# Optimization experiments

Measured on AMD Instinct MI355X. Metric: run time of the kernel, lower is better.

## Reference

```python
import jax, jax.numpy as jnp
import numpy as np

HIDDEN = 2048
N_HEADS = 16
HEAD_DIM = HIDDEN // N_HEADS
ROPE_THETA = 10000.0
BSZ, SEQ = 2, 2048
NEG_INF = -1e9


def setup_inputs() -> dict:
    key = jax.random.key(0)
    ks = jax.random.split(key, 5)
    scale = 1.0 / np.sqrt(HIDDEN)
    hidden_states = jax.random.normal(ks[0], (BSZ, SEQ, HIDDEN), dtype=jnp.float32)
    Wq = jax.random.normal(ks[1], (HIDDEN, HIDDEN), dtype=jnp.float32) * scale
    Wk = jax.random.normal(ks[2], (HIDDEN, HIDDEN), dtype=jnp.float32) * scale
    Wv = jax.random.normal(ks[3], (HIDDEN, HIDDEN), dtype=jnp.float32) * scale
    Wo = jax.random.normal(ks[4], (HIDDEN, HIDDEN), dtype=jnp.float32) * scale
    # additive causal mask, [1, 1, S, S]
    causal = jnp.triu(jnp.full((SEQ, SEQ), NEG_INF, dtype=jnp.float32), k=1)
    attention_mask = causal[None, None, :, :]
    position_ids = jnp.arange(SEQ, dtype=jnp.int32)
    return {
        "hidden_states": hidden_states,
        "Wq": Wq, "Wk": Wk, "Wv": Wv, "Wo": Wo,
        "attention_mask": attention_mask,
        "position_ids": position_ids,
    }


def _rotate_half(x):
    half = x.shape[-1] // 2
    return jnp.concatenate((-x[..., half:], x[..., :half]), axis=-1)


def _rope_tables(seq_len, position_ids):
    # inv_freq: [head_dim/2]
    inv_freq = 1.0 / (ROPE_THETA ** (jnp.arange(0, HEAD_DIM, 2, dtype=jnp.float32) / HEAD_DIM))
    t = jnp.arange(seq_len, dtype=jnp.float32)
    freqs = t[:, None] * inv_freq[None, :]              # [S, D/2]
    emb = jnp.concatenate((freqs, freqs), axis=-1)      # [S, D]
    cos = jnp.cos(emb)[position_ids]                    # [S, D]
    sin = jnp.sin(emb)[position_ids]
    return cos, sin


def reference(hidden_states, Wq, Wk, Wv, Wo, attention_mask, position_ids):
    b, s, h = hidden_states.shape
    def proj(W):
        return (hidden_states @ W.T).reshape(b, s, N_HEADS, HEAD_DIM).transpose(0, 2, 1, 3)
    q = proj(Wq)  # [B, H, S, D]
    k = proj(Wk)
    v = proj(Wv)
    cos, sin = _rope_tables(s, position_ids)            # [S, D], broadcasts over B,H
    q = q * cos + _rotate_half(q) * sin
    k = k * cos + _rotate_half(k) * sin
    scores = jnp.einsum('bhqd,bhkd->bhqk', q, k) / np.sqrt(HEAD_DIM)
    scores = scores + attention_mask
    w = jax.nn.softmax(scores, axis=-1)
    out = jnp.einsum('bhqk,bhkd->bhqd', w, v)           # [B, H, S, D]
    out = out.transpose(0, 2, 1, 3).reshape(b, s, h)
    return out @ Wo.T
```

## Files before the change

kernel.cpp:

```cpp
#include <hip/hip_runtime.h>
#include <cstdint>
#include <cstddef>

typedef __bf16 bf16;
typedef __bf16 bf16x4 __attribute__((ext_vector_type(4)));
typedef __bf16 bf16x8 __attribute__((ext_vector_type(8)));
typedef float  f32x4  __attribute__((ext_vector_type(4)));
typedef short  s16x4  __attribute__((ext_vector_type(4)));

#define HIDDEN 2048
#define NHEADS 16
#define HDIM   128
#define BSZ    2
#define SEQ    2048
#define BS     (BSZ*SEQ)
#define QKW    (2*HIDDEN)

union b4u { bf16x4 h; s16x4 s; };

__device__ __forceinline__ void async16(const bf16* g, bf16* l) {
    __builtin_amdgcn_global_load_lds(
        (const __attribute__((address_space(1))) unsigned int*)g,
        (__attribute__((address_space(3))) unsigned int*)l, 16, 0, 0);
}

__global__ __launch_bounds__(256) void cast_all(const float* __restrict__ hs,
                                                const float* __restrict__ Wq,
                                                const float* __restrict__ Wk,
                                                const float* __restrict__ Wv,
                                                const float* __restrict__ Wo,
                                                const int* __restrict__ pos,
                                                bf16* __restrict__ hs_b,
                                                bf16* __restrict__ wqkv,
                                                bf16* __restrict__ wo_b,
                                                float2* __restrict__ tab) {
    int i = blockIdx.x * 256 + threadIdx.x;
    if (i >= 6291456) {
        int j = i - 6291456;
        int s = j >> 6, p = j & 63;
        float t = (float)pos[s];
        float inv = expf(-(float)(2 * p) * (9.2103403719761836f / 128.0f));
        float sn, cs;
        sincosf(t * inv, &sn, &cs);
        tab[j] = make_float2(cs, sn);
        return;
    }
    const float* src; bf16* dst; int off;
    if (i < 2097152) { src = hs; dst = hs_b; off = i; }
    else {
        int j = i - 2097152;
        int r = j >> 20;
        off = j & 1048575;
        if      (r == 0) { src = Wq; dst = wqkv; }
        else if (r == 1) { src = Wk; dst = wqkv + (size_t)4194304; }
        else if (r == 2) { src = Wv; dst = wqkv + (size_t)8388608; }
        else             { src = Wo; dst = wo_b; }
    }
    const float4 v = ((const float4*)src)[off];
    bf16x4 o;
    o.x = (bf16)v.x; o.y = (bf16)v.y; o.z = (bf16)v.z; o.w = (bf16)v.w;
    ((bf16x4*)dst)[off] = o;
}

__global__ __launch_bounds__(256) void gemm_qkv(const bf16* __restrict__ A,
                                                const bf16* __restrict__ Bt,
                                                const float2* __restrict__ tab,
                                                bf16* __restrict__ qk,
                                                bf16* __restrict__ vtb) {
    __shared__ bf16 Als[128 * 32];
    __shared__ bf16 Bls[128 * 32];
    const int K    = HIDDEN;
    const int tid  = threadIdx.x;
    const int lane = tid & 63;
    const int w    = tid >> 6;
    const int l15  = lane & 15;
    const int quad = lane >> 4;
    const int mTile = blockIdx.y * 128;
    const int nTile = blockIdx.x * 128;
    const int wm = (w >> 1) * 64;
    const int wv = w & 1;

    f32x4 acc[4][4];
#pragma unroll
    for (int i = 0; i < 4; ++i)
#pragma unroll
        for (int j = 0; j < 4; ++j) acc[i][j] = (f32x4){0.f, 0.f, 0.f, 0.f};

    const bf16* gA = A + (size_t)(mTile + w * 32 + (lane >> 2)) * K + (lane & 3) * 8;
    const bf16* gB = Bt + (size_t)(nTile + w * 32 + (lane >> 2)) * K + (lane & 3) * 8;
    bf16* lA = Als + w * 1024;
    bf16* lB = Bls + w * 1024;

    for (int k0 = 0; k0 < K; k0 += 32) {
        async16(gA + k0,          lA);
        async16(gA + 16 * K + k0, lA + 512);
        async16(gB + k0,          lB);
        async16(gB + 16 * K + k0, lB + 512);
        __syncthreads();

        bf16x8 af[4], bfr[4];
#pragma unroll
        for (int mi = 0; mi < 4; ++mi)
            af[mi] = *(const bf16x8*)(Als + (wm + mi * 16 + l15) * 32 + quad * 8);
#pragma unroll
        for (int ni = 0; ni < 4; ++ni) {
            int co = wv * 32 + (ni & 1) * 16 + (ni >> 1) * 64;
            bfr[ni] = *(const bf16x8*)(Bls + (co + l15) * 32 + quad * 8);
        }
#pragma unroll
        for (int mi = 0; mi < 4; ++mi)
#pragma unroll
            for (int ni = 0; ni < 4; ++ni)
                acc[mi][ni] = __builtin_amdgcn_mfma_f32_16x16x32_bf16(
                    af[mi], bfr[ni], acc[mi][ni], 0, 0, 0);
        __syncthreads();
    }

    if (nTile < QKW) {
#pragma unroll
        for (int mi = 0; mi < 4; ++mi)
#pragma unroll
            for (int r = 0; r < 4; ++r) {
                int row = mTile + wm + mi * 16 + quad * 4 + r;
                int s   = row & (SEQ - 1);
                float2 t0 = tab[s * 64 + wv * 32 + l15];
                float2 t1 = tab[s * 64 + wv * 32 + 16 + l15];
                size_t rb = (size_t)row * QKW + nTile + wv * 32 + l15;
                float lo0 = acc[mi][0][r], hi0 = acc[mi][2][r];
                float lo1 = acc[mi][1][r], hi1 = acc[mi][3][r];
                qk[rb]      = (bf16)(lo0 * t0.x - hi0 * t0.y);
                qk[rb + 64] = (bf16)(hi0 * t0.x + lo0 * t0.y);
                qk[rb + 16] = (bf16)(lo1 * t1.x - hi1 * t1.y);
                qk[rb + 80] = (bf16)(hi1 * t1.x + lo1 * t1.y);
            }
    } else {
#pragma unroll
        for (int mi = 0; mi < 4; ++mi)
#pragma unroll
            for (int ni = 0; ni < 4; ++ni) {
                int col_v = (nTile - QKW) + wv * 32 + (ni & 1) * 16 + (ni >> 1) * 64 + l15;
                int row0  = mTile + wm + mi * 16 + quad * 4;
                bf16x4 pk;
#pragma unroll
                for (int r = 0; r < 4; ++r) pk[r] = (bf16)acc[mi][ni][r];
                *(bf16x4*)(vtb + (size_t)col_v * BS + row0) = pk;
            }
    }
}

template <typename OutT>
__global__ __launch_bounds__(256) void gemm_bt(const bf16* __restrict__ A,
                                               const bf16* __restrict__ Bt,
                                               OutT* __restrict__ C,
                                               int M, int N, int K) {
    __shared__ bf16 Als[128 * 32];
    __shared__ bf16 Bls[128 * 32];
    const int tid  = threadIdx.x;
    const int lane = tid & 63;
    const int w    = tid >> 6;
    const int l15  = lane & 15;
    const int quad = lane >> 4;
    const int mTile = blockIdx.y * 128;
    const int nTile = blockIdx.x * 128;
    const int wm = (w >> 1) * 64;
    const int wn = (w & 1) * 64;

    f32x4 acc[4][4];
#pragma unroll
    for (int i = 0; i < 4; ++i)
#pragma unroll
        for (int j = 0; j < 4; ++j) acc[i][j] = (f32x4){0.f, 0.f, 0.f, 0.f};

    const bf16* gA = A + (size_t)(mTile + w * 32 + (lane >> 2)) * K + (lane & 3) * 8;
    const bf16* gB = Bt + (size_t)(nTile + w * 32 + (lane >> 2)) * K + (lane & 3) * 8;
    bf16* lA = Als + w * 1024;
    bf16* lB = Bls + w * 1024;

    for (int k0 = 0; k0 < K; k0 += 32) {
        async16(gA + k0,          lA);
        async16(gA + 16 * K + k0, lA + 512);
        async16(gB + k0,          lB);
        async16(gB + 16 * K + k0, lB + 512);
        __syncthreads();

        bf16x8 af[4], bfr[4];
#pragma unroll
        for (int mi = 0; mi < 4; ++mi)
            af[mi] = *(const bf16x8*)(Als + (wm + mi * 16 + l15) * 32 + quad * 8);
#pragma unroll
        for (int ni = 0; ni < 4; ++ni)
            bfr[ni] = *(const bf16x8*)(Bls + (wn + ni * 16 + l15) * 32 + quad * 8);
#pragma unroll
        for (int mi = 0; mi < 4; ++mi)
#pragma unroll
            for (int ni = 0; ni < 4; ++ni)
                acc[mi][ni] = __builtin_amdgcn_mfma_f32_16x16x32_bf16(
                    af[mi], bfr[ni], acc[mi][ni], 0, 0, 0);
        __syncthreads();
    }

#pragma unroll
    for (int mi = 0; mi < 4; ++mi)
#pragma unroll
        for (int ni = 0; ni < 4; ++ni)
#pragma unroll
            for (int r = 0; r < 4; ++r) {
                int row = mTile + wm + mi * 16 + quad * 4 + r;
                int col = nTile + wn + ni * 16 + l15;
                C[(size_t)row * N + col] = (OutT)acc[mi][ni][r];
            }
}

__global__ __launch_bounds__(256) void attn_kernel(const bf16* __restrict__ qk,
                                                   const bf16* __restrict__ vt,
                                                   bf16* __restrict__ ao) {
    __shared__ bf16 Kls[64 * 128];
    __shared__ bf16 Vls[128 * 64];

    const int tid  = threadIdx.x;
    const int lane = tid & 63;
    const int w    = tid >> 6;
    const int l15  = lane & 15;
    const int quad = lane >> 4;
    const int bid  = blockIdx.x;
    const int qt   = 31 - (bid >> 5);
    const int bh   = bid & 31;
    const int b    = bh >> 4;
    const int h    = bh & 15;
    const int qbase = qt * 64;
    const size_t seq0 = (size_t)b * SEQ;

    bf16x8 qf[4];
    {
        const bf16* qp = qk + (seq0 + qbase + w * 16 + l15) * QKW + h * HDIM + quad * 8;
#pragma unroll
        for (int ks = 0; ks < 4; ++ks) qf[ks] = *(const bf16x8*)(qp + ks * 32);
    }

    f32x4 o[8];
#pragma unroll
    for (int i = 0; i < 8; ++i) o[i] = (f32x4){0.f, 0.f, 0.f, 0.f};
    float m_s = -3e38f, l_s = 0.f;
    const int qg = qbase + w * 16 + l15;

    const int krow = lane >> 4;
    const int kp   = lane & 15;
    const int vrow = lane >> 3;
    const int vp   = lane & 7;
    const int sw   = l15 & 7;

    for (int t = 0; t <= qt; ++t) {
        const int kb = t * 64;
#pragma unroll
        for (int i = 0; i < 4; ++i) {
            int j = w * 16 + i * 4 + krow;
            int c = (kp & 8) | ((kp & 7) ^ (j & 7));
            async16(qk + (seq0 + kb + j) * QKW + HIDDEN + h * HDIM + c * 8,
                    Kls + (w * 4 + i) * 512);
        }
#pragma unroll
        for (int i = 0; i < 4; ++i) {
            int d = w * 32 + i * 8 + vrow;
            int c = vp ^ (d & 7);
            async16(vt + (size_t)(h * HDIM + d) * (size_t)BS + seq0 + kb + c * 8,
                    Vls + (w * 4 + i) * 512);
        }
        __syncthreads();

        f32x4 sa[4];
#pragma unroll
        for (int ni = 0; ni < 4; ++ni) sa[ni] = (f32x4){0.f, 0.f, 0.f, 0.f};
#pragma unroll
        for (int ni = 0; ni < 4; ++ni)
#pragma unroll
            for (int ks = 0; ks < 4; ++ks) {
                bf16x8 kf = *(const bf16x8*)(Kls + (ni * 16 + l15) * 128 +
                                             (((ks * 4 + quad) ^ sw) << 3));
                sa[ni] = __builtin_amdgcn_mfma_f32_16x16x32_bf16(kf, qf[ks], sa[ni], 0, 0, 0);
            }

        const float scale = 0.08838834764831845f * 1.4426950408889634f;
        float rmax = -3e38f;
        const bool diag = (t == qt);
#pragma unroll
        for (int ni = 0; ni < 4; ++ni)
#pragma unroll
            for (int r = 0; r < 4; ++r) {
                float sv = sa[ni][r] * scale;
                if (diag) {
                    int jg = kb + ni * 16 + quad * 4 + r;
                    if (jg > qg) sv = -1e30f;
                }
                sa[ni][r] = sv;
                rmax = fmaxf(rmax, sv);
            }
        rmax = fmaxf(rmax, __shfl_xor(rmax, 16));
        rmax = fmaxf(rmax, __shfl_xor(rmax, 32));

        float mn = fmaxf(m_s, rmax);
        float alpha = exp2f(m_s - mn);
        m_s = mn;
        float rsum = 0.f;
        b4u pb[4];
#pragma unroll
        for (int ni = 0; ni < 4; ++ni)
#pragma unroll
            for (int r = 0; r < 4; ++r) {
                float e = exp2f(sa[ni][r] - mn);
                rsum += e;
                pb[ni].h[r] = (bf16)e;
            }
        rsum += __shfl_xor(rsum, 16);
        rsum += __shfl_xor(rsum, 32);
        l_s = l_s * alpha + rsum;

        if (__ballot(alpha != 1.f) != 0ull) {
#pragma unroll
            for (int n2 = 0; n2 < 8; ++n2)
#pragma unroll
                for (int r = 0; r < 4; ++r) o[n2][r] *= alpha;
        }

#pragma unroll
        for (int n2 = 0; n2 < 8; ++n2)
#pragma unroll
            for (int ni = 0; ni < 4; ++ni) {
                b4u vf;
                vf.h = *(const bf16x4*)(Vls + (n2 * 16 + l15) * 64 +
                                        ((((ni * 2 + (quad >> 1)) ^ sw) << 3) + (quad & 1) * 4));
                o[n2] = __builtin_amdgcn_mfma_f32_16x16x16bf16_1k(vf.s, pb[ni].s, o[n2], 0, 0, 0);
            }
        __syncthreads();
    }

    const float inv = 1.0f / l_s;
    bf16* op = ao + (seq0 + qg) * HIDDEN + h * HDIM + quad * 4;
#pragma unroll
    for (int n2 = 0; n2 < 8; ++n2) {
        bf16x4 pk;
#pragma unroll
        for (int r = 0; r < 4; ++r) pk[r] = (bf16)(o[n2][r] * inv);
        *(bf16x4*)(op + n2 * 16) = pk;
    }
}

extern "C" void kernel_launch(void* const* d_in, const int* in_sizes, int n_in,
                              void* d_out, int out_size, void* d_ws, size_t ws_size,
                              hipStream_t stream) {
    const float* hs = (const float*)d_in[0];
    const float* Wq = (const float*)d_in[1];
    const float* Wk = (const float*)d_in[2];
    const float* Wv = (const float*)d_in[3];
    const float* Wo = (const float*)d_in[4];
    const int* pos  = (const int*)d_in[6];
    float* out = (float*)d_out;

    bf16* hs_b = (bf16*)d_ws;
    bf16* wqkv = hs_b + (size_t)8388608;
    bf16* wo_b = wqkv + (size_t)12582912;
    bf16* qkb  = wo_b + (size_t)4194304;
    bf16* vtb  = qkb + (size_t)16777216;
    bf16* ao   = vtb + (size_t)8388608;
    float2* tab = (float2*)ao;

    cast_all<<<25088, 256, 0, stream>>>(hs, Wq, Wk, Wv, Wo, pos, hs_b, wqkv, wo_b, tab);
    gemm_qkv<<<dim3(48, 32), 256, 0, stream>>>(hs_b, wqkv, tab, qkb, vtb);
    attn_kernel<<<1024, 256, 0, stream>>>(qkb, vtb, ao);
    gemm_bt<float><<<dim3(HIDDEN / 128, BS / 128), 256, 0, stream>>>(ao, wo_b, out, BS, HIDDEN, HIDDEN);
}
```

Before: 398.8 us.

## Double GEMM K-tile with XOR-swizzled LDS; use 128-query attention blocks with 8 waves

Both GEMM kernels now stage 64-wide K slices instead of 32. The LDS layout is XOR-swizzled to avoid bank conflicts, which halves the number of barrier round-trips per output tile. The attention kernel moves from 64 to 128 query rows per block with 512 threads, so each K/V tile loaded into LDS is shared by twice as many queries. Waves whose rows lie fully above a key tile skip its compute but still take part in loads and barriers. The trade-off is more LDS per GEMM block and more idle waves on diagonal tiles in attention, which may reduce occupancy.

New measurement: 403.9 us. About the same (+1.3%).

```diff
diff --git a/kernel.cpp b/kernel.cpp
--- a/kernel.cpp
+++ b/kernel.cpp
@@ -62,19 +62,21 @@
     ((bf16x4*)dst)[off] = o;
 }
 
+
 __global__ __launch_bounds__(256) void gemm_qkv(const bf16* __restrict__ A,
                                                 const bf16* __restrict__ Bt,
                                                 const float2* __restrict__ tab,
                                                 bf16* __restrict__ qk,
                                                 bf16* __restrict__ vtb) {
-    __shared__ bf16 Als[128 * 32];
-    __shared__ bf16 Bls[128 * 32];
+    __shared__ bf16 Als[128 * 64];
+    __shared__ bf16 Bls[128 * 64];
     const int K    = HIDDEN;
     const int tid  = threadIdx.x;
     const int lane = tid & 63;
     const int w    = tid >> 6;
     const int l15  = lane & 15;
     const int quad = lane >> 4;
+    const int sw   = l15 & 7;
     const int mTile = blockIdx.y * 128;
     const int nTile = blockIdx.x * 128;
     const int wm = (w >> 1) * 64;
@@ -86,33 +88,40 @@
 #pragma unroll
         for (int j = 0; j < 4; ++j) acc[i][j] = (f32x4){0.f, 0.f, 0.f, 0.f};
 
-    const bf16* gA = A + (size_t)(mTile + w * 32 + (lane >> 2)) * K + (lane & 3) * 8;
-    const bf16* gB = Bt + (size_t)(nTile + w * 32 + (lane >> 2)) * K + (lane & 3) * 8;
-    bf16* lA = Als + w * 1024;
-    bf16* lB = Bls + w * 1024;
-
-    for (int k0 = 0; k0 < K; k0 += 32) {
-        async16(gA + k0,          lA);
-        async16(gA + 16 * K + k0, lA + 512);
-        async16(gB + k0,          lB);
-        async16(gB + 16 * K + k0, lB + 512);
-        __syncthreads();
-
-        bf16x8 af[4], bfr[4];
-#pragma unroll
-        for (int mi = 0; mi < 4; ++mi)
-            af[mi] = *(const bf16x8*)(Als + (wm + mi * 16 + l15) * 32 + quad * 8);
-#pragma unroll
-        for (int ni = 0; ni < 4; ++ni) {
-            int co = wv * 32 + (ni & 1) * 16 + (ni >> 1) * 64;
-            bfr[ni] = *(const bf16x8*)(Bls + (co + l15) * 32 + quad * 8);
-        }
-#pragma unroll
-        for (int mi = 0; mi < 4; ++mi)
-#pragma unroll
-            for (int ni = 0; ni < 4; ++ni)
-                acc[mi][ni] = __builtin_amdgcn_mfma_f32_16x16x32_bf16(
-                    af[mi], bfr[ni], acc[mi][ni], 0, 0, 0);
+    const int cOff = (((lane & 7) ^ (lane >> 3)) & 7) * 8;
+    const bf16* gA = A + (size_t)(mTile + w * 32 + (lane >> 3)) * K + cOff;
+    const bf16* gB = Bt + (size_t)(nTile + w * 32 + (lane >> 3)) * K + cOff;
+    bf16* lA = Als + w * 2048;
+    bf16* lB = Bls + w * 2048;
+    const int rstep = 8 * K;
+
+    for (int k0 = 0; k0 < K; k0 += 64) {
+#pragma unroll
+        for (int i = 0; i < 4; ++i) async16(gA + k0 + i * rstep, lA + i * 512);
+#pragma unroll
+        for (int i = 0; i < 4; ++i) async16(gB + k0 + i * rstep, lB + i * 512);
+        __syncthreads();
+
+#pragma unroll
+        for (int s = 0; s < 2; ++s) {
+            bf16x8 af[4], bfr[4];
+#pragma unroll
+            for (int mi = 0; mi < 4; ++mi)
+                af[mi] = *(const bf16x8*)(Als + (wm + mi * 16 + l15) * 64 +
+                                          (((s * 4 + quad) ^ sw) << 3));
+#pragma unroll
+            for (int ni = 0; ni < 4; ++ni) {
+                int co = wv * 32 + (ni & 1) * 16 + (ni >> 1) * 64;
+                bfr[ni] = *(const bf16x8*)(Bls + (co + l15) * 64 +
+                                           (((s * 4 + quad) ^ sw) << 3));
+            }
+#pragma unroll
+            for (int mi = 0; mi < 4; ++mi)
+#pragma unroll
+                for (int ni = 0; ni < 4; ++ni)
+                    acc[mi][ni] = __builtin_amdgcn_mfma_f32_16x16x32_bf16(
+                        af[mi], bfr[ni], acc[mi][ni], 0, 0, 0);
+        }
         __syncthreads();
     }
 
@@ -153,13 +162,14 @@
                                                const bf16* __restrict__ Bt,
                                                OutT* __restrict__ C,
                                                int M, int N, int K) {
-    __shared__ bf16 Als[128 * 32];
-    __shared__ bf16 Bls[128 * 32];
+    __shared__ bf16 Als[128 * 64];
+    __shared__ bf16 Bls[128 * 64];
     const int tid  = threadIdx.x;
     const int lane = tid & 63;
     const int w    = tid >> 6;
     const int l15  = lane & 15;
     const int quad = lane >> 4;
+    const int sw   = l15 & 7;
     const int mTile = blockIdx.y * 128;
     const int nTile = blockIdx.x * 128;
     const int wm = (w >> 1) * 64;
@@ -171,31 +181,38 @@
 #pragma unroll
         for (int j = 0; j < 4; ++j) acc[i][j] = (f32x4){0.f, 0.f, 0.f, 0.f};
 
-    const bf16* gA = A + (size_t)(mTile + w * 32 + (lane >> 2)) * K + (lane & 3) * 8;
-    const bf16* gB = Bt + (size_t)(nTile + w * 32 + (lane >> 2)) * K + (lane & 3) * 8;
-    bf16* lA = Als + w * 1024;
-    bf16* lB = Bls + w * 1024;
-
-    for (int k0 = 0; k0 < K; k0 += 32) {
-        async16(gA + k0,          lA);
-        async16(gA + 16 * K + k0, lA + 512);
-        async16(gB + k0,          lB);
-        async16(gB + 16 * K + k0, lB + 512);
-        __syncthreads();
-
-        bf16x8 af[4], bfr[4];
-#pragma unroll
-        for (int mi = 0; mi < 4; ++mi)
-            af[mi] = *(const bf16x8*)(Als + (wm + mi * 16 + l15) * 32 + quad * 8);
-#pragma unroll
-        for (int ni = 0; ni < 4; ++ni)
-            bfr[ni] = *(const bf16x8*)(Bls + (wn + ni * 16 + l15) * 32 + quad * 8);
-#pragma unroll
-        for (int mi = 0; mi < 4; ++mi)
+    const int cOff = (((lane & 7) ^ (lane >> 3)) & 7) * 8;
+    const bf16* gA = A + (size_t)(mTile + w * 32 + (lane >> 3)) * K + cOff;
+    const bf16* gB = Bt + (size_t)(nTile + w * 32 + (lane >> 3)) * K + cOff;
+    bf16* lA = Als + w * 2048;
+    bf16* lB = Bls + w * 2048;
+    const int rstep = 8 * K;
+
+    for (int k0 = 0; k0 < K; k0 += 64) {
+#pragma unroll
+        for (int i = 0; i < 4; ++i) async16(gA + k0 + i * rstep, lA + i * 512);
+#pragma unroll
+        for (int i = 0; i < 4; ++i) async16(gB + k0 + i * rstep, lB + i * 512);
+        __syncthreads();
+
+#pragma unroll
+        for (int s = 0; s < 2; ++s) {
+            bf16x8 af[4], bfr[4];
+#pragma unroll
+            for (int mi = 0; mi < 4; ++mi)
+                af[mi] = *(const bf16x8*)(Als + (wm + mi * 16 + l15) * 64 +
+                                          (((s * 4 + quad) ^ sw) << 3));
 #pragma unroll
             for (int ni = 0; ni < 4; ++ni)
-                acc[mi][ni] = __builtin_amdgcn_mfma_f32_16x16x32_bf16(
-                    af[mi], bfr[ni], acc[mi][ni], 0, 0, 0);
+                bfr[ni] = *(const bf16x8*)(Bls + (wn + ni * 16 + l15) * 64 +
+                                           (((s * 4 + quad) ^ sw) << 3));
+#pragma unroll
+            for (int mi = 0; mi < 4; ++mi)
+#pragma unroll
+                for (int ni = 0; ni < 4; ++ni)
+                    acc[mi][ni] = __builtin_amdgcn_mfma_f32_16x16x32_bf16(
+                        af[mi], bfr[ni], acc[mi][ni], 0, 0, 0);
+        }
         __syncthreads();
     }
 
@@ -211,7 +228,7 @@
             }
 }
 
-__global__ __launch_bounds__(256) void attn_kernel(const bf16* __restrict__ qk,
+__global__ __launch_bounds__(512) void attn_kernel(const bf16* __restrict__ qk,
                                                    const bf16* __restrict__ vt,
                                                    bf16* __restrict__ ao) {
     __shared__ bf16 Kls[64 * 128];
@@ -223,11 +240,11 @@
     const int l15  = lane & 15;
     const int quad = lane >> 4;
     const int bid  = blockIdx.x;
-    const int qt   = 31 - (bid >> 5);
+    const int qt   = 15 - (bid >> 5);
     const int bh   = bid & 31;
     const int b    = bh >> 4;
     const int h    = bh & 15;
-    const int qbase = qt * 64;
+    const int qbase = qt * 128;
     const size_t seq0 = (size_t)b * SEQ;
 
     bf16x8 qf[4];
@@ -242,94 +259,95 @@
     for (int i = 0; i < 8; ++i) o[i] = (f32x4){0.f, 0.f, 0.f, 0.f};
     float m_s = -3e38f, l_s = 0.f;
     const int qg = qbase + w * 16 + l15;
-
-    const int krow = lane >> 4;
+    const int wmin = qbase + w * 16;
+
     const int kp   = lane & 15;
-    const int vrow = lane >> 3;
-    const int vp   = lane & 7;
     const int sw   = l15 & 7;
-
-    for (int t = 0; t <= qt; ++t) {
+    const int tmax = 2 * qt + 1;
+
+    for (int t = 0; t <= tmax; ++t) {
         const int kb = t * 64;
 #pragma unroll
-        for (int i = 0; i < 4; ++i) {
-            int j = w * 16 + i * 4 + krow;
+        for (int i = 0; i < 2; ++i) {
+            int j = (w * 2 + i) * 4 + (lane >> 4);
             int c = (kp & 8) | ((kp & 7) ^ (j & 7));
             async16(qk + (seq0 + kb + j) * QKW + HIDDEN + h * HDIM + c * 8,
-                    Kls + (w * 4 + i) * 512);
-        }
-#pragma unroll
-        for (int i = 0; i < 4; ++i) {
-            int d = w * 32 + i * 8 + vrow;
-            int c = vp ^ (d & 7);
+                    Kls + (w * 2 + i) * 512);
+        }
+#pragma unroll
+        for (int i = 0; i < 2; ++i) {
+            int d = (w * 2 + i) * 8 + (lane >> 3);
+            int c = (lane & 7) ^ (d & 7);
             async16(vt + (size_t)(h * HDIM + d) * (size_t)BS + seq0 + kb + c * 8,
-                    Vls + (w * 4 + i) * 512);
-        }
-        __syncthreads();
-
-        f32x4 sa[4];
-#pragma unroll
-        for (int ni = 0; ni < 4; ++ni) sa[ni] = (f32x4){0.f, 0.f, 0.f, 0.f};
-#pragma unroll
-        for (int ni = 0; ni < 4; ++ni)
-#pragma unroll
-            for (int ks = 0; ks < 4; ++ks) {
-                bf16x8 kf = *(const bf16x8*)(Kls + (ni * 16 + l15) * 128 +
-                                             (((ks * 4 + quad) ^ sw) << 3));
-                sa[ni] = __builtin_amdgcn_mfma_f32_16x16x32_bf16(kf, qf[ks], sa[ni], 0, 0, 0);
-            }
-
-        const float scale = 0.08838834764831845f * 1.4426950408889634f;
-        float rmax = -3e38f;
-        const bool diag = (t == qt);
-#pragma unroll
-        for (int ni = 0; ni < 4; ++ni)
-#pragma unroll
-            for (int r = 0; r < 4; ++r) {
-                float sv = sa[ni][r] * scale;
-                if (diag) {
-                    int jg = kb + ni * 16 + quad * 4 + r;
-                    if (jg > qg) sv = -1e30f;
+                    Vls + (w * 2 + i) * 512);
+        }
+        __syncthreads();
+
+        if (kb <= wmin + 15) {
+            f32x4 sa[4];
+#pragma unroll
+            for (int ni = 0; ni < 4; ++ni) sa[ni] = (f32x4){0.f, 0.f, 0.f, 0.f};
+#pragma unroll
+            for (int ni = 0; ni < 4; ++ni)
+#pragma unroll
+                for (int ks = 0; ks < 4; ++ks) {
+                    bf16x8 kf = *(const bf16x8*)(Kls + (ni * 16 + l15) * 128 +
+                                                 (((ks * 4 + quad) ^ sw) << 3));
+                    sa[ni] = __builtin_amdgcn_mfma_f32_16x16x32_bf16(kf, qf[ks], sa[ni], 0, 0, 0);
                 }
-                sa[ni][r] = sv;
-                rmax = fmaxf(rmax, sv);
-            }
-        rmax = fmaxf(rmax, __shfl_xor(rmax, 16));
-        rmax = fmaxf(rmax, __shfl_xor(rmax, 32));
-
-        float mn = fmaxf(m_s, rmax);
-        float alpha = exp2f(m_s - mn);
-        m_s = mn;
-        float rsum = 0.f;
-        b4u pb[4];
-#pragma unroll
-        for (int ni = 0; ni < 4; ++ni)
-#pragma unroll
-            for (int r = 0; r < 4; ++r) {
-                float e = exp2f(sa[ni][r] - mn);
-                rsum += e;
-                pb[ni].h[r] = (bf16)e;
-            }
-        rsum += __shfl_xor(rsum, 16);
-        rsum += __shfl_xor(rsum, 32);
-        l_s = l_s * alpha + rsum;
-
-        if (__ballot(alpha != 1.f) != 0ull) {
+
+            const float scale = 0.08838834764831845f * 1.4426950408889634f;
+            float rmax = -3e38f;
+            const bool diag = (kb + 63 > wmin);
+#pragma unroll
+            for (int ni = 0; ni < 4; ++ni)
+#pragma unroll
+                for (int r = 0; r < 4; ++r) {
+                    float sv = sa[ni][r] * scale;
+                    if (diag) {
+                        int jg = kb + ni * 16 + quad * 4 + r;
+                        if (jg > qg) sv = -1e30f;
+                    }
+                    sa[ni][r] = sv;
+                    rmax = fmaxf(rmax, sv);
+                }
+            rmax = fmaxf(rmax, __shfl_xor(rmax, 16));
+            rmax = fmaxf(rmax, __shfl_xor(rmax, 32));
+
+            float mn = fmaxf(m_s, rmax);
+            float alpha = exp2f(m_s - mn);
+            m_s = mn;
+            float rsum = 0.f;
+            b4u pb[4];
+#pragma unroll
+            for (int ni = 0; ni < 4; ++ni)
+#pragma unroll
+                for (int r = 0; r < 4; ++r) {
+                    float e = exp2f(sa[ni][r] - mn);
+                    rsum += e;
+                    pb[ni].h[r] = (bf16)e;
+                }
+            rsum += __shfl_xor(rsum, 16);
+            rsum += __shfl_xor(rsum, 32);
+            l_s = l_s * alpha + rsum;
+
+            if (__ballot(alpha != 1.f) != 0ull) {
+#pragma unroll
+                for (int n2 = 0; n2 < 8; ++n2)
+#pragma unroll
+                    for (int r = 0; r < 4; ++r) o[n2][r] *= alpha;
+            }
+
 #pragma unroll
             for (int n2 = 0; n2 < 8; ++n2)
 #pragma unroll
-                for (int r = 0; r < 4; ++r) o[n2][r] *= alpha;
-        }
-
-#pragma unroll
-        for (int n2 = 0; n2 < 8; ++n2)
-#pragma unroll
-            for (int ni = 0; ni < 4; ++ni) {
-                b4u vf;
-                vf.h = *(const bf16x4*)(Vls + (n2 * 16 + l15) * 64 +
-                                        ((((ni * 2 + (quad >> 1)) ^ sw) << 3) + (quad & 1) * 4));
-                o[n2] = __builtin_amdgcn_mfma_f32_16x16x16bf16_1k(vf.s, pb[ni].s, o[n2], 0, 0, 0);
-            }
+                for (int ni = 0; ni < 4; ++ni) {
+                    b4u vf;
+                    vf.h = *(const bf16x4*)(Vls + (n2 * 16 + l15) * 64 +
+                                            ((((ni * 2 + (quad >> 1)) ^ sw) << 3) + (quad & 1) * 4));
+                    o[n2] = __builtin_amdgcn_mfma_f32_16x16x16bf16_1k(vf.s, pb[ni].s, o[n2], 0, 0, 0);
+                }
+        }
         __syncthreads();
     }
 
@@ -365,6 +383,6 @@
 
     cast_all<<<25088, 256, 0, stream>>>(hs, Wq, Wk, Wv, Wo, pos, hs_b, wqkv, wo_b, tab);
     gemm_qkv<<<dim3(48, 32), 256, 0, stream>>>(hs_b, wqkv, tab, qkb, vtb);
-    attn_kernel<<<1024, 256, 0, stream>>>(qkb, vtb, ao);
+    attn_kernel<<<512, 512, 0, stream>>>(qkb, vtb, ao);
     gemm_bt<float><<<dim3(HIDDEN / 128, BS / 128), 256, 0, stream>>>(ao, wo_b, out, BS, HIDDEN, HIDDEN);
 }
```
